# Kernel optimization log

Measured on AMD Instinct MI355X. Metric: run time of the kernel, lower is better.

## Reference

```python
import jax, jax.numpy as jnp
import numpy as np
import math

B, T, C = 4, 2048, 1024
H, D = 16, 64  # n_head, head_dim; H*D == C

def setup_inputs() -> dict:
    key = jax.random.key(0)
    ks = jax.random.split(key, 8)
    s = 1.0 / math.sqrt(C)
    return {
        "x": jax.random.normal(ks[0], (B, T, C), jnp.float32),
        "W_attn": jax.random.normal(ks[1], (C, 3 * C), jnp.float32) * s,
        "b_attn": jax.random.normal(ks[2], (3 * C,), jnp.float32) * 0.02,
        "W_proj": jax.random.normal(ks[3], (C, C), jnp.float32) * s,
        "b_proj": jax.random.normal(ks[4], (C,), jnp.float32) * 0.02,
        "bQ": jax.random.normal(ks[5], (H, D), jnp.float32) * 0.02,
        "bK": jax.random.normal(ks[6], (H, D), jnp.float32) * 0.02,
        "bV": jax.random.normal(ks[7], (H, D), jnp.float32) * 0.02,
    }

def reference(x, W_attn, b_attn, W_proj, b_proj, bQ, bK, bV):
    Bx, Tx, Cx = x.shape
    qkv = x @ W_attn + b_attn                       # [B,T,3C]
    q, k, v = jnp.split(qkv, 3, axis=-1)
    def heads(t):
        return t.reshape(Bx, Tx, H, D).transpose(0, 2, 1, 3)  # [B,H,T,D]
    q = heads(q) + bQ[None, :, None, :]
    k = heads(k) + bK[None, :, None, :]
    v = heads(v) + bV[None, :, None, :]
    scale = 1.0 / math.sqrt(D)
    scores = jnp.einsum('bhqd,bhkd->bhqk', q, k) * scale      # [B,H,T,T]
    causal = jnp.tril(jnp.ones((Tx, Tx), dtype=bool))
    scores = jnp.where(causal[None, None], scores, -jnp.inf)
    att = jax.nn.softmax(scores, axis=-1)
    y = jnp.einsum('bhqk,bhkd->bhqd', att, v)                 # [B,H,T,D]
    y = y.transpose(0, 2, 1, 3).reshape(Bx, Tx, Cx)
    return y @ W_proj + b_proj
```

## Files before the change

kernel.cpp:

```cpp
#include <hip/hip_runtime.h>
#include <hip/hip_bf16.h>

#define BB 4
#define TT 2048
#define CC 1024
#define HH 16
#define DD 64

typedef __bf16 bf16x8 __attribute__((ext_vector_type(8)));
typedef float f32x4 __attribute__((ext_vector_type(4)));
typedef unsigned int u32x4 __attribute__((ext_vector_type(4)));
typedef unsigned int u32x2 __attribute__((ext_vector_type(2)));
typedef unsigned short u16x8 __attribute__((ext_vector_type(8)));
typedef unsigned short u16x4 __attribute__((ext_vector_type(4)));
typedef unsigned int u32;

__device__ __forceinline__ unsigned short f2bf(float f) {
  u32 u = __builtin_bit_cast(u32, f);
  u += 0x7fff + ((u >> 16) & 1);
  return (unsigned short)(u >> 16);
}

__device__ __forceinline__ bf16x8 lds_load8(const unsigned short* p) {
  u32x4 t = *(const u32x4*)p;
  return __builtin_bit_cast(bf16x8, t);
}

__device__ __forceinline__ void g2l16(const unsigned short* g, unsigned short* l) {
  __builtin_amdgcn_global_load_lds(
      (const __attribute__((address_space(1))) u32*)g,
      (__attribute__((address_space(3))) u32*)l, 16, 0, 0);
}

__device__ __forceinline__ void drain_then_sync() {
  __builtin_amdgcn_s_waitcnt(0);
  __syncthreads();
}

__global__ __launch_bounds__(256) void prep(
    const float* __restrict__ x, const float* __restrict__ Wa,
    const float* __restrict__ Wp, unsigned short* __restrict__ xb,
    unsigned short* __restrict__ Wta, unsigned short* __restrict__ Wtp)
{
  __shared__ unsigned short T[64 * 68];
  const int tid = threadIdx.x;
  const int bid = blockIdx.x;
  if (bid < 4096) {
    int i = (bid * 256 + tid) * 8;
    f32x4 a = *(const f32x4*)(x + i);
    f32x4 b = *(const f32x4*)(x + i + 4);
    u16x8 o;
    o[0] = f2bf(a[0]); o[1] = f2bf(a[1]); o[2] = f2bf(a[2]); o[3] = f2bf(a[3]);
    o[4] = f2bf(b[0]); o[5] = f2bf(b[1]); o[6] = f2bf(b[2]); o[7] = f2bf(b[3]);
    *(u16x8*)(xb + i) = o;
    return;
  }
  const float* W; unsigned short* Wt; int N, n0, k0;
  if (bid < 4096 + 768) {
    int b2 = bid - 4096;  W = Wa; Wt = Wta; N = 3072;
    n0 = (b2 % 48) * 64;  k0 = (b2 / 48) * 64;
  } else {
    int b2 = bid - 4864;  W = Wp; Wt = Wtp; N = 1024;
    n0 = (b2 % 16) * 64;  k0 = (b2 / 16) * 64;
  }
#pragma unroll
  for (int it = 0; it < 4; ++it) {
    int idx = it * 256 + tid;
    int kk = idx >> 4, nn = (idx & 15) * 4;
    f32x4 v = *(const f32x4*)(W + (size_t)(k0 + kk) * N + n0 + nn);
    u16x4 p;
    p[0] = f2bf(v[0]); p[1] = f2bf(v[1]); p[2] = f2bf(v[2]); p[3] = f2bf(v[3]);
    *(u16x4*)(&T[kk * 68 + nn]) = p;
  }
  __syncthreads();
#pragma unroll
  for (int it = 0; it < 4; ++it) {
    int idx = it * 256 + tid;
    int nn = idx >> 4, kc = (idx & 15) * 4;
    u16x4 o;
    o[0] = T[(kc + 0) * 68 + nn];
    o[1] = T[(kc + 1) * 68 + nn];
    o[2] = T[(kc + 2) * 68 + nn];
    o[3] = T[(kc + 3) * 68 + nn];
    *(u16x4*)(Wt + (size_t)(n0 + nn) * 1024 + k0 + kc) = o;
  }
}

__global__ __launch_bounds__(256) void qkv_gemm(
    const unsigned short* __restrict__ xb, const unsigned short* __restrict__ Wt,
    const float* __restrict__ b_attn, const float* __restrict__ bQ,
    const float* __restrict__ bK, const float* __restrict__ bV,
    unsigned short* __restrict__ Qb, unsigned short* __restrict__ Kb,
    unsigned short* __restrict__ Vb)
{
  __shared__ unsigned short Al[128 * 64];
  __shared__ unsigned short Bl[128 * 64];
  const int tid = threadIdx.x;
  const int w = tid >> 6, lane = tid & 63;
  const int l16 = lane & 15, quad = lane >> 4;
  const int nblk = blockIdx.x % 24, mblk = blockIdx.x / 24;
  const int m0 = mblk * 128, n0 = nblk * 128;
  const int wm = (w & 1) * 64, wn = (w >> 1) * 64;

  const int srow = lane >> 3;
  const int schunk = ((lane & 7) ^ (srow & 7)) * 8;
  const unsigned short* ga = xb + (size_t)(m0 + w * 8 + srow) * 1024 + schunk;
  const unsigned short* gb = Wt + (size_t)(n0 + w * 8 + srow) * 1024 + schunk;
  unsigned short* la = &Al[(w * 8) * 64];
  unsigned short* lb = &Bl[(w * 8) * 64];

  f32x4 acc[4][4] = {};

  for (int kb = 0; kb < 1024; kb += 64) {
    drain_then_sync();
#pragma unroll
    for (int i = 0; i < 4; ++i) {
      g2l16(ga + kb + (size_t)i * 32 * 1024, la + i * 32 * 64);
      g2l16(gb + kb + (size_t)i * 32 * 1024, lb + i * 32 * 64);
    }
    drain_then_sync();
    bf16x8 af[4][2], bfr[4][2];
#pragma unroll
    for (int mi = 0; mi < 4; ++mi)
#pragma unroll
      for (int dk = 0; dk < 2; ++dk)
        af[mi][dk] = lds_load8(
            &Al[(wm + mi * 16 + l16) * 64 + (((dk * 4 + quad) ^ (l16 & 7)) * 8)]);
#pragma unroll
    for (int ni = 0; ni < 4; ++ni)
#pragma unroll
      for (int dk = 0; dk < 2; ++dk)
        bfr[ni][dk] = lds_load8(
            &Bl[(wn + ni * 16 + l16) * 64 + (((dk * 4 + quad) ^ (l16 & 7)) * 8)]);
#pragma unroll
    for (int mi = 0; mi < 4; ++mi)
#pragma unroll
      for (int ni = 0; ni < 4; ++ni) {
        acc[mi][ni] = __builtin_amdgcn_mfma_f32_16x16x32_bf16(
            af[mi][0], bfr[ni][0], acc[mi][ni], 0, 0, 0);
        acc[mi][ni] = __builtin_amdgcn_mfma_f32_16x16x32_bf16(
            af[mi][1], bfr[ni][1], acc[mi][ni], 0, 0, 0);
      }
  }

  unsigned short* dst[4];
  float biasv[4], sc[4];
  int st[4];
#pragma unroll
  for (int ni = 0; ni < 4; ++ni) {
    int col = n0 + wn + ni * 16 + l16;
    int sec = col >> 10, cc = col & 1023;
    const float* hb = (sec == 0) ? bQ : (sec == 1 ? bK : bV);
    biasv[ni] = b_attn[col] + hb[cc];
    sc[ni] = (sec == 0) ? 0.125f * 1.44269504f : 1.0f;
    if (sec == 2) {
      dst[ni] = Vb + (size_t)(cc >> 6) * (DD * TT) + (size_t)(cc & 63) * TT;
      st[ni] = 1;
    } else {
      unsigned short* base = (sec == 0) ? Qb : Kb;
      dst[ni] = base + (size_t)(cc >> 6) * (TT * DD) + (cc & 63);
      st[ni] = 64;
    }
  }
#pragma unroll
  for (int mi = 0; mi < 4; ++mi)
#pragma unroll
    for (int r = 0; r < 4; ++r) {
      int m = m0 + wm + mi * 16 + quad * 4 + r;
      int bidx = m >> 11, t = m & 2047;
      size_t co = (size_t)bidx * (HH * TT * DD);
#pragma unroll
      for (int ni = 0; ni < 4; ++ni)
        dst[ni][co + (size_t)t * st[ni]] = f2bf((acc[mi][ni][r] + biasv[ni]) * sc[ni]);
    }
}

__global__ __launch_bounds__(256) void attn_kernel(
    const unsigned short* __restrict__ Qb, const unsigned short* __restrict__ Kb,
    const unsigned short* __restrict__ Vtg, unsigned short* __restrict__ Yb)
{
  __shared__ unsigned short Kl[64 * 64];
  __shared__ unsigned short Vl[64 * 64];
  __shared__ unsigned short Pl[4 * 32 * 72];
  const int tid = threadIdx.x;
  const int w = tid >> 6, lane = tid & 63;
  const int l16 = lane & 15, quad = lane >> 4;
  const int qt = 15 - (blockIdx.x >> 6);
  const int bh = blockIdx.x & 63;
  const int b = bh >> 4, h = bh & 15;
  const int q0 = qt * 128, qw = q0 + w * 32;

  const unsigned short* Qg = Qb + (size_t)bh * TT * DD;
  const unsigned short* Kg = Kb + (size_t)bh * TT * DD;
  const unsigned short* Vg = Vtg + (size_t)bh * DD * TT;

  bf16x8 qf[2][2];
#pragma unroll
  for (int mi = 0; mi < 2; ++mi)
#pragma unroll
    for (int dk = 0; dk < 2; ++dk) {
      u32x4 t = *(const u32x4*)(Qg + (size_t)(qw + mi * 16 + l16) * 64 + dk * 32 + quad * 8);
      qf[mi][dk] = __builtin_bit_cast(bf16x8, t);
    }

  f32x4 accO[2][4] = {};
  f32x4 accL[2] = {};
  u16x8 o16;
#pragma unroll
  for (int j = 0; j < 8; ++j) o16[j] = 0x3F80;
  const bf16x8 onesf = __builtin_bit_cast(bf16x8, o16);

  const int srow = w * 8 + (lane >> 3);
  const int schunk = ((lane & 7) ^ (srow & 7)) * 8;
  const int kkey = 4 * (srow & 15) + (srow >> 4);
  const unsigned short* gk1 = Kg + (size_t)kkey * 64 + schunk;
  const unsigned short* gk2 = Kg + (size_t)(kkey + 2) * 64 + schunk;
  const unsigned short* gv1 = Vg + (size_t)srow * TT + schunk;
  const unsigned short* gv2 = Vg + (size_t)(srow + 32) * TT + schunk;
  unsigned short* klw = &Kl[w * 512];
  unsigned short* vlw = &Vl[w * 512];

  const int kend = q0 + 64;
  for (int k0 = 0; k0 <= kend; k0 += 64) {
    drain_then_sync();
    g2l16(gk1 + (size_t)k0 * 64, klw);
    g2l16(gk2 + (size_t)k0 * 64, klw + 2048);
    g2l16(gv1 + k0, vlw);
    g2l16(gv2 + k0, vlw + 2048);
    drain_then_sync();
    if (k0 > qw + 31) continue;

    f32x4 accS[2][4] = {};
#pragma unroll
    for (int ni = 0; ni < 4; ++ni)
#pragma unroll
      for (int dk = 0; dk < 2; ++dk) {
        bf16x8 kf = lds_load8(
            &Kl[(ni * 16 + l16) * 64 + (((dk * 4 + quad) ^ (l16 & 7)) * 8)]);
#pragma unroll
        for (int mi = 0; mi < 2; ++mi)
          accS[mi][ni] = __builtin_amdgcn_mfma_f32_16x16x32_bf16(
              qf[mi][dk], kf, accS[mi][ni], 0, 0, 0);
      }

    const bool maskT = (k0 + 63 > qw);
#pragma unroll
    for (int mi = 0; mi < 2; ++mi)
#pragma unroll
      for (int r = 0; r < 4; ++r) {
        int qrow = qw + mi * 16 + quad * 4 + r;
        float s0 = accS[mi][0][r], s1 = accS[mi][1][r];
        float s2 = accS[mi][2][r], s3 = accS[mi][3][r];
        if (maskT) {
          int kb = k0 + 4 * l16;
          if (kb + 0 > qrow) s0 = -3e38f;
          if (kb + 1 > qrow) s1 = -3e38f;
          if (kb + 2 > qrow) s2 = -3e38f;
          if (kb + 3 > qrow) s3 = -3e38f;
        }
        u32 e0 = __builtin_bit_cast(u32, exp2f(s0));
        u32 e1 = __builtin_bit_cast(u32, exp2f(s1));
        u32 e2 = __builtin_bit_cast(u32, exp2f(s2));
        u32 e3 = __builtin_bit_cast(u32, exp2f(s3));
        u32x2 pv;
        pv[0] = __builtin_amdgcn_perm(e1, e0, 0x07060302);
        pv[1] = __builtin_amdgcn_perm(e3, e2, 0x07060302);
        *(u32x2*)(&Pl[(w * 32 + mi * 16 + quad * 4 + r) * 72 + 4 * l16]) = pv;
      }

#pragma unroll
    for (int kc = 0; kc < 2; ++kc) {
      bf16x8 pf[2];
#pragma unroll
      for (int mi = 0; mi < 2; ++mi)
        pf[mi] = lds_load8(&Pl[(w * 32 + mi * 16 + l16) * 72 + kc * 32 + quad * 8]);
#pragma unroll
      for (int dn = 0; dn < 4; ++dn) {
        bf16x8 vf = lds_load8(
            &Vl[(dn * 16 + l16) * 64 + (((kc * 4 + quad) ^ (l16 & 7)) * 8)]);
#pragma unroll
        for (int mi = 0; mi < 2; ++mi)
          accO[mi][dn] = __builtin_amdgcn_mfma_f32_16x16x32_bf16(
              pf[mi], vf, accO[mi][dn], 0, 0, 0);
      }
#pragma unroll
      for (int mi = 0; mi < 2; ++mi)
        accL[mi] = __builtin_amdgcn_mfma_f32_16x16x32_bf16(
            pf[mi], onesf, accL[mi], 0, 0, 0);
    }
  }

#pragma unroll
  for (int mi = 0; mi < 2; ++mi)
#pragma unroll
    for (int r = 0; r < 4; ++r) {
      int q = qw + mi * 16 + quad * 4 + r;
      float inv = 1.0f / accL[mi][r];
      size_t base = ((size_t)b * TT + q) * CC + h * DD;
#pragma unroll
      for (int dn = 0; dn < 4; ++dn)
        Yb[base + dn * 16 + l16] = f2bf(accO[mi][dn][r] * inv);
    }
}

__global__ __launch_bounds__(256) void proj_gemm(
    const unsigned short* __restrict__ Yb, const unsigned short* __restrict__ Wt,
    const float* __restrict__ bp, float* __restrict__ out)
{
  __shared__ unsigned short Al[128 * 64];
  __shared__ unsigned short Bl[128 * 64];
  const int tid = threadIdx.x;
  const int w = tid >> 6, lane = tid & 63;
  const int l16 = lane & 15, quad = lane >> 4;
  const int nblk = blockIdx.x & 7, mblk = blockIdx.x >> 3;
  const int m0 = mblk * 128, n0 = nblk * 128;
  const int wm = (w & 1) * 64, wn = (w >> 1) * 64;

  const int srow = lane >> 3;
  const int schunk = ((lane & 7) ^ (srow & 7)) * 8;
  const unsigned short* ga = Yb + (size_t)(m0 + w * 8 + srow) * 1024 + schunk;
  const unsigned short* gb = Wt + (size_t)(n0 + w * 8 + srow) * 1024 + schunk;
  unsigned short* la = &Al[(w * 8) * 64];
  unsigned short* lb = &Bl[(w * 8) * 64];

  f32x4 acc[4][4] = {};

  for (int kb = 0; kb < 1024; kb += 64) {
    drain_then_sync();
#pragma unroll
    for (int i = 0; i < 4; ++i) {
      g2l16(ga + kb + (size_t)i * 32 * 1024, la + i * 32 * 64);
      g2l16(gb + kb + (size_t)i * 32 * 1024, lb + i * 32 * 64);
    }
    drain_then_sync();
    bf16x8 af[4][2], bfr[4][2];
#pragma unroll
    for (int mi = 0; mi < 4; ++mi)
#pragma unroll
      for (int dk = 0; dk < 2; ++dk)
        af[mi][dk] = lds_load8(
            &Al[(wm + mi * 16 + l16) * 64 + (((dk * 4 + quad) ^ (l16 & 7)) * 8)]);
#pragma unroll
    for (int ni = 0; ni < 4; ++ni)
#pragma unroll
      for (int dk = 0; dk < 2; ++dk)
        bfr[ni][dk] = lds_load8(
            &Bl[(wn + ni * 16 + l16) * 64 + (((dk * 4 + quad) ^ (l16 & 7)) * 8)]);
#pragma unroll
    for (int mi = 0; mi < 4; ++mi)
#pragma unroll
      for (int ni = 0; ni < 4; ++ni) {
        acc[mi][ni] = __builtin_amdgcn_mfma_f32_16x16x32_bf16(
            af[mi][0], bfr[ni][0], acc[mi][ni], 0, 0, 0);
        acc[mi][ni] = __builtin_amdgcn_mfma_f32_16x16x32_bf16(
            af[mi][1], bfr[ni][1], acc[mi][ni], 0, 0, 0);
      }
  }

#pragma unroll
  for (int mi = 0; mi < 4; ++mi)
#pragma unroll
    for (int r = 0; r < 4; ++r) {
      int m = m0 + wm + mi * 16 + quad * 4 + r;
#pragma unroll
      for (int ni = 0; ni < 4; ++ni) {
        int c = n0 + wn + ni * 16 + l16;
        out[(size_t)m * 1024 + c] = acc[mi][ni][r] + bp[c];
      }
    }
}

extern "C" void kernel_launch(void* const* d_in, const int* in_sizes, int n_in,
                              void* d_out, int out_size, void* d_ws, size_t ws_size,
                              hipStream_t stream) {
  const float* x      = (const float*)d_in[0];
  const float* W_attn = (const float*)d_in[1];
  const float* b_attn = (const float*)d_in[2];
  const float* W_proj = (const float*)d_in[3];
  const float* b_proj = (const float*)d_in[4];
  const float* bQ     = (const float*)d_in[5];
  const float* bK     = (const float*)d_in[6];
  const float* bV     = (const float*)d_in[7];
  float* out = (float*)d_out;

  unsigned short* xb   = (unsigned short*)d_ws;
  unsigned short* Yb   = xb;
  unsigned short* Wt_a = xb + 8388608;
  unsigned short* Wt_p = Wt_a + 3145728;
  unsigned short* Qb   = Wt_p + 1048576;
  unsigned short* Kb   = Qb + 8388608;
  unsigned short* Vb   = Kb + 8388608;

  prep<<<dim3(4096 + 768 + 256), dim3(256), 0, stream>>>(x, W_attn, W_proj,
                                                         xb, Wt_a, Wt_p);
  qkv_gemm<<<dim3(64 * 24), dim3(256), 0, stream>>>(xb, Wt_a, b_attn, bQ, bK, bV,
                                                    Qb, Kb, Vb);
  attn_kernel<<<dim3(16 * 64), dim3(256), 0, stream>>>(Qb, Kb, Vb, Yb);
  proj_gemm<<<dim3(64 * 8), dim3(256), 0, stream>>>(Yb, Wt_p, b_proj, out);
}
```

Baseline: 284.5 us.

## Double-buffer B tiles in LDS and prefetch A operands into registers in GEMMs

Both the QKV and projection GEMMs now load the A operand directly from global memory into registers, bypassing LDS, and double-buffer it across phases. The B (weight) tile is double-buffered in LDS so the next k-step's async copy is issued before the current step's MFMAs, which drops one barrier per iteration. The aim is to overlap global loads with compute and remove the load-then-wait serialization. In exchange, register pressure rises and A reads become per-lane 16-byte loads duplicated across the two waves sharing rows.

```diff
diff --git a/kernel.cpp b/kernel.cpp
--- a/kernel.cpp
+++ b/kernel.cpp
@@ -93,8 +93,7 @@
     unsigned short* __restrict__ Qb, unsigned short* __restrict__ Kb,
     unsigned short* __restrict__ Vb)
 {
-  __shared__ unsigned short Al[128 * 64];
-  __shared__ unsigned short Bl[128 * 64];
+  __shared__ unsigned short Bl[2][128 * 64];
   const int tid = threadIdx.x;
   const int w = tid >> 6, lane = tid & 63;
   const int l16 = lane & 15, quad = lane >> 4;
@@ -104,43 +103,60 @@
 
   const int srow = lane >> 3;
   const int schunk = ((lane & 7) ^ (srow & 7)) * 8;
-  const unsigned short* ga = xb + (size_t)(m0 + w * 8 + srow) * 1024 + schunk;
   const unsigned short* gb = Wt + (size_t)(n0 + w * 8 + srow) * 1024 + schunk;
-  unsigned short* la = &Al[(w * 8) * 64];
-  unsigned short* lb = &Bl[(w * 8) * 64];
+  const unsigned short* ga = xb + (size_t)(m0 + wm + l16) * 1024 + quad * 8;
 
   f32x4 acc[4][4] = {};
-
-  for (int kb = 0; kb < 1024; kb += 64) {
-    drain_then_sync();
-#pragma unroll
-    for (int i = 0; i < 4; ++i) {
-      g2l16(ga + kb + (size_t)i * 32 * 1024, la + i * 32 * 64);
-      g2l16(gb + kb + (size_t)i * 32 * 1024, lb + i * 32 * 64);
-    }
-    drain_then_sync();
-    bf16x8 af[4][2], bfr[4][2];
-#pragma unroll
-    for (int mi = 0; mi < 4; ++mi)
-#pragma unroll
-      for (int dk = 0; dk < 2; ++dk)
-        af[mi][dk] = lds_load8(
-            &Al[(wm + mi * 16 + l16) * 64 + (((dk * 4 + quad) ^ (l16 & 7)) * 8)]);
-#pragma unroll
-    for (int ni = 0; ni < 4; ++ni)
-#pragma unroll
-      for (int dk = 0; dk < 2; ++dk)
-        bfr[ni][dk] = lds_load8(
-            &Bl[(wn + ni * 16 + l16) * 64 + (((dk * 4 + quad) ^ (l16 & 7)) * 8)]);
-#pragma unroll
-    for (int mi = 0; mi < 4; ++mi)
-#pragma unroll
-      for (int ni = 0; ni < 4; ++ni) {
-        acc[mi][ni] = __builtin_amdgcn_mfma_f32_16x16x32_bf16(
-            af[mi][0], bfr[ni][0], acc[mi][ni], 0, 0, 0);
-        acc[mi][ni] = __builtin_amdgcn_mfma_f32_16x16x32_bf16(
-            af[mi][1], bfr[ni][1], acc[mi][ni], 0, 0, 0);
-      }
+  u32x4 aA[8], aB[8];
+
+#pragma unroll
+  for (int i = 0; i < 4; ++i)
+    g2l16(gb + (size_t)i * 32 * 1024, &Bl[0][(w * 8 + i * 32) * 64]);
+#pragma unroll
+  for (int mi = 0; mi < 4; ++mi)
+#pragma unroll
+    for (int dk = 0; dk < 2; ++dk)
+      aA[mi * 2 + dk] = *(const u32x4*)(ga + (size_t)mi * 16 * 1024 + dk * 32);
+
+#pragma unroll 1
+  for (int kb = 0; kb < 1024; kb += 128) {
+#pragma unroll
+    for (int ph = 0; ph < 2; ++ph) {
+      const int cur = ph;
+      const int kc_ = kb + ph * 64;
+      const int kn = kc_ + 64;
+      drain_then_sync();
+      if (kn < 1024) {
+#pragma unroll
+        for (int i = 0; i < 4; ++i)
+          g2l16(gb + kn + (size_t)i * 32 * 1024, &Bl[1 - cur][(w * 8 + i * 32) * 64]);
+      }
+      bf16x8 bfr[4][2];
+#pragma unroll
+      for (int ni = 0; ni < 4; ++ni)
+#pragma unroll
+        for (int dk = 0; dk < 2; ++dk)
+          bfr[ni][dk] = lds_load8(
+              &Bl[cur][(wn + ni * 16 + l16) * 64 + (((dk * 4 + quad) ^ (l16 & 7)) * 8)]);
+      u32x4* acur = (ph == 0) ? aA : aB;
+      u32x4* anxt = (ph == 0) ? aB : aA;
+      if (kn < 1024) {
+#pragma unroll
+        for (int mi = 0; mi < 4; ++mi)
+#pragma unroll
+          for (int dk = 0; dk < 2; ++dk)
+            anxt[mi * 2 + dk] = *(const u32x4*)(ga + (size_t)mi * 16 * 1024 + kn + dk * 32);
+      }
+#pragma unroll
+      for (int mi = 0; mi < 4; ++mi)
+#pragma unroll
+        for (int ni = 0; ni < 4; ++ni) {
+          acc[mi][ni] = __builtin_amdgcn_mfma_f32_16x16x32_bf16(
+              __builtin_bit_cast(bf16x8, acur[mi * 2 + 0]), bfr[ni][0], acc[mi][ni], 0, 0, 0);
+          acc[mi][ni] = __builtin_amdgcn_mfma_f32_16x16x32_bf16(
+              __builtin_bit_cast(bf16x8, acur[mi * 2 + 1]), bfr[ni][1], acc[mi][ni], 0, 0, 0);
+        }
+    }
   }
 
   unsigned short* dst[4];
@@ -307,8 +323,7 @@
     const unsigned short* __restrict__ Yb, const unsigned short* __restrict__ Wt,
     const float* __restrict__ bp, float* __restrict__ out)
 {
-  __shared__ unsigned short Al[128 * 64];
-  __shared__ unsigned short Bl[128 * 64];
+  __shared__ unsigned short Bl[2][128 * 64];
   const int tid = threadIdx.x;
   const int w = tid >> 6, lane = tid & 63;
   const int l16 = lane & 15, quad = lane >> 4;
@@ -318,43 +333,59 @@
 
   const int srow = lane >> 3;
   const int schunk = ((lane & 7) ^ (srow & 7)) * 8;
-  const unsigned short* ga = Yb + (size_t)(m0 + w * 8 + srow) * 1024 + schunk;
   const unsigned short* gb = Wt + (size_t)(n0 + w * 8 + srow) * 1024 + schunk;
-  unsigned short* la = &Al[(w * 8) * 64];
-  unsigned short* lb = &Bl[(w * 8) * 64];
+  const unsigned short* ga = Yb + (size_t)(m0 + wm + l16) * 1024 + quad * 8;
 
   f32x4 acc[4][4] = {};
-
-  for (int kb = 0; kb < 1024; kb += 64) {
-    drain_then_sync();
-#pragma unroll
-    for (int i = 0; i < 4; ++i) {
-      g2l16(ga + kb + (size_t)i * 32 * 1024, la + i * 32 * 64);
-      g2l16(gb + kb + (size_t)i * 32 * 1024, lb + i * 32 * 64);
-    }
-    drain_then_sync();
-    bf16x8 af[4][2], bfr[4][2];
-#pragma unroll
-    for (int mi = 0; mi < 4; ++mi)
-#pragma unroll
-      for (int dk = 0; dk < 2; ++dk)
-        af[mi][dk] = lds_load8(
-            &Al[(wm + mi * 16 + l16) * 64 + (((dk * 4 + quad) ^ (l16 & 7)) * 8)]);
-#pragma unroll
-    for (int ni = 0; ni < 4; ++ni)
-#pragma unroll
-      for (int dk = 0; dk < 2; ++dk)
-        bfr[ni][dk] = lds_load8(
-            &Bl[(wn + ni * 16 + l16) * 64 + (((dk * 4 + quad) ^ (l16 & 7)) * 8)]);
-#pragma unroll
-    for (int mi = 0; mi < 4; ++mi)
-#pragma unroll
-      for (int ni = 0; ni < 4; ++ni) {
-        acc[mi][ni] = __builtin_amdgcn_mfma_f32_16x16x32_bf16(
-            af[mi][0], bfr[ni][0], acc[mi][ni], 0, 0, 0);
-        acc[mi][ni] = __builtin_amdgcn_mfma_f32_16x16x32_bf16(
-            af[mi][1], bfr[ni][1], acc[mi][ni], 0, 0, 0);
-      }
+  u32x4 aA[8], aB[8];
+
+#pragma unroll
+  for (int i = 0; i < 4; ++i)
+    g2l16(gb + (size_t)i * 32 * 1024, &Bl[0][(w * 8 + i * 32) * 64]);
+#pragma unroll
+  for (int mi = 0; mi < 4; ++mi)
+#pragma unroll
+    for (int dk = 0; dk < 2; ++dk)
+      aA[mi * 2 + dk] = *(const u32x4*)(ga + (size_t)mi * 16 * 1024 + dk * 32);
+
+#pragma unroll 1
+  for (int kb = 0; kb < 1024; kb += 128) {
+#pragma unroll
+    for (int ph = 0; ph < 2; ++ph) {
+      const int cur = ph;
+      const int kn = kb + ph * 64 + 64;
+      drain_then_sync();
+      if (kn < 1024) {
+#pragma unroll
+        for (int i = 0; i < 4; ++i)
+          g2l16(gb + kn + (size_t)i * 32 * 1024, &Bl[1 - cur][(w * 8 + i * 32) * 64]);
+      }
+      bf16x8 bfr[4][2];
+#pragma unroll
+      for (int ni = 0; ni < 4; ++ni)
+#pragma unroll
+        for (int dk = 0; dk < 2; ++dk)
+          bfr[ni][dk] = lds_load8(
+              &Bl[cur][(wn + ni * 16 + l16) * 64 + (((dk * 4 + quad) ^ (l16 & 7)) * 8)]);
+      u32x4* acur = (ph == 0) ? aA : aB;
+      u32x4* anxt = (ph == 0) ? aB : aA;
+      if (kn < 1024) {
+#pragma unroll
+        for (int mi = 0; mi < 4; ++mi)
+#pragma unroll
+          for (int dk = 0; dk < 2; ++dk)
+            anxt[mi * 2 + dk] = *(const u32x4*)(ga + (size_t)mi * 16 * 1024 + kn + dk * 32);
+      }
+#pragma unroll
+      for (int mi = 0; mi < 4; ++mi)
+#pragma unroll
+        for (int ni = 0; ni < 4; ++ni) {
+          acc[mi][ni] = __builtin_amdgcn_mfma_f32_16x16x32_bf16(
+              __builtin_bit_cast(bf16x8, acur[mi * 2 + 0]), bfr[ni][0], acc[mi][ni], 0, 0, 0);
+          acc[mi][ni] = __builtin_amdgcn_mfma_f32_16x16x32_bf16(
+              __builtin_bit_cast(bf16x8, acur[mi * 2 + 1]), bfr[ni][1], acc[mi][ni], 0, 0, 0);
+        }
+    }
   }
 
 #pragma unroll
```

Measured after the change: 347.3 us. +22.1%, slower.
